# Optimization experiments

Measured on AMD Instinct MI355X. Metric: run time of the kernel, lower is better.

The kernel has to match this reference:

```python
import jax, jax.numpy as jnp
import numpy as np

V0, V1, V2 = 2000, 1500, 500   # diag / proc / med vocab sizes
D = 256                        # emb_dim
T = 16                         # visits per patient (query and memory)
P = 512                        # memory-bank patients
LD, LP, LM = 24, 16, 24        # codes per visit per type
PAD = V0 + V1 + V2             # padding row index (zeroed)
THRESH = 0.8
EPS = 1e-6


def setup_inputs() -> dict:
    key = jax.random.key(0)
    ks = jax.random.split(key, 16)
    inp = {
        "q_diag": jax.random.randint(ks[0], (T, LD), 0, V0),
        "q_proc": jax.random.randint(ks[1], (T, LP), 0, V1),
        "q_med": jax.random.randint(ks[2], (T, LM), 0, V2),
        "mem_diag": jax.random.randint(ks[3], (P, T, LD), 0, V0),
        "mem_proc": jax.random.randint(ks[4], (P, T, LP), 0, V1),
        "mem_med": jax.random.randint(ks[5], (P, T, LM), 0, V2),
        "emb": (jax.random.normal(ks[6], (PAD + 1, D)) * 0.05).at[PAD].set(0.0),
        "Wih": jax.random.normal(ks[7], (3 * D, D)) * 0.05,
        "Whh": jax.random.normal(ks[8], (3 * D, D)) * 0.05,
        "bih": jax.random.normal(ks[9], (3 * D,)) * 0.05,
        "bhh": jax.random.normal(ks[10], (3 * D,)) * 0.05,
        "W2": jax.random.normal(ks[11], (D, D)) * 0.05,
        "b2": jax.random.normal(ks[12], (D,)) * 0.05,
        "Wo": jax.random.normal(ks[13], (V2, D)) * 0.05,
        "bo": jax.random.normal(ks[14], (V2,)) * 0.05,
        "k": 16,
    }
    return inp


def _run_gru(x, Wih, Whh, bih, bhh):
    # x: [B, T, D]; torch nn.GRU gate order: r, z, n
    xT = jnp.swapaxes(x, 0, 1)                      # [T, B, D]
    gx = xT @ Wih.T + bih                           # [T, B, 3D]
    h0 = jnp.zeros(x.shape[:1] + x.shape[2:], x.dtype)  # [B, D]

    def step(h, gx_t):
        gh = h @ Whh.T + bhh
        xr, xz, xn = jnp.split(gx_t, 3, axis=-1)
        hr, hz, hn = jnp.split(gh, 3, axis=-1)
        r = jax.nn.sigmoid(xr + hr)
        z = jax.nn.sigmoid(xz + hz)
        n = jnp.tanh(xn + r * hn)
        h_new = (1.0 - z) * n + z * h
        return h_new, h_new

    _, hs = jax.lax.scan(step, h0, gx)
    return jnp.swapaxes(hs, 0, 1)                   # [B, T, D]


def _encode_visits(diag, proc, med, emb, Wih, Whh, bih, bhh, W2, b2):
    # diag/proc/med: [B, T, L*] int. Returns encoders for visits 1..T-1: [B, T-1, D].
    e_d = emb[diag].sum(axis=2)                     # [B, T, D]
    e_p = emb[proc + V0].sum(axis=2)
    e_m = emb[med + V0 + V1].sum(axis=2)
    e_nomed = e_d + e_p                             # current visit excludes meds
    e_full = e_nomed + e_m                          # history visits include meds
    h = _run_gru(e_full, Wih, Whh, bih, bhh)        # [B, T, D]
    # attn_g = softmax over size-1 axis == 1 exactly, so encoder_1 drops out.
    terms = jnp.tanh(h @ W2.T + b2) * e_full        # [B, T, D]
    c = jnp.cumsum(terms, axis=1)                   # prefix context sums
    return c[:, :-1] + e_nomed[:, 1:]               # enc_i = c_{i-1..} + current_i


def reference(q_diag, q_proc, q_med, mem_diag, mem_proc, mem_med,
              emb, Wih, Whh, bih, bhh, W2, b2, Wo, bo, k):
    gru = (Wih, Whh, bih, bhh)
    # Memory bank: every prefix encoder of every memory patient -> [P*(T-1), D]
    M = _encode_visits(mem_diag, mem_proc, mem_med, emb, *gru, W2, b2)
    M = M.reshape(-1, D)
    # Query patient prefix encoders -> [T-1, D]
    Q = _encode_visits(q_diag[None], q_proc[None], q_med[None], emb, *gru, W2, b2)[0]
    # Cosine similarity (torch CosineSimilarity, eps=1e-6)
    qn = jnp.maximum(jnp.linalg.norm(Q, axis=-1, keepdims=True), EPS)
    mn = jnp.maximum(jnp.linalg.norm(M, axis=-1, keepdims=True), EPS)
    sims = (Q / qn) @ (M / mn).T                    # [T-1, Nmem]
    vals, idx = jax.lax.top_k(sims, k)              # [T-1, k]
    w = jnp.where(vals > THRESH, vals, 0.0)         # threshold mask
    gathered = M[idx]                               # [T-1, k, D]
    out = Q + jnp.einsum("qk,qkd->qd", w, gathered) # weighted gather-sum
    return jax.nn.sigmoid(out @ Wo.T + bo)          # [T-1, V2]
```

## Files before the change

kernel.cpp:

```cpp
#include <hip/hip_runtime.h>
#include <math.h>

constexpr int V0_ = 2000, V1_ = 1500, V2_ = 500;
constexpr int D_ = 256, T_ = 16, P_ = 512;
constexpr int LD_ = 24, LP_ = 16, LM_ = 24;
constexpr int NPAT = P_ + 1;
constexpr int NV   = NPAT * T_;
constexpr int NM   = P_ * (T_ - 1);
constexpr int NQ   = T_ - 1;
constexpr int NROWS = NPAT * NQ;
constexpr float THRESH_ = 0.8f;
constexpr float EPS_ = 1e-6f;

__device__ __forceinline__ float sigmoidf_(float x) { return 1.0f / (1.0f + expf(-x)); }

#define BLO(u) __uint_as_float((u) << 16)
#define BHI(u) __uint_as_float((u) & 0xffff0000u)

__global__ void embed_kernel(const int* __restrict__ qd, const int* __restrict__ qp,
                             const int* __restrict__ qm, const int* __restrict__ md,
                             const int* __restrict__ mp, const int* __restrict__ mm,
                             const float* __restrict__ emb,
                             float* __restrict__ e_nomed, float* __restrict__ e_full) {
  int b = blockIdx.x;
  int p = b / T_, t = b % T_;
  int tid = threadIdx.x;
  __shared__ int codes[64];
  if (tid < 64) {
    int c;
    if (tid < LD_) {
      c = (p < P_) ? md[(p * T_ + t) * LD_ + tid] : qd[t * LD_ + tid];
    } else if (tid < LD_ + LP_) {
      int i = tid - LD_;
      c = ((p < P_) ? mp[(p * T_ + t) * LP_ + i] : qp[t * LP_ + i]) + V0_;
    } else {
      int i = tid - LD_ - LP_;
      c = ((p < P_) ? mm[(p * T_ + t) * LM_ + i] : qm[t * LM_ + i]) + V0_ + V1_;
    }
    codes[tid] = c;
  }
  __syncthreads();
  float s0 = 0.f, s1 = 0.f;
  #pragma unroll 8
  for (int i = 0; i < LD_ + LP_; ++i) s0 += emb[codes[i] * D_ + tid];
  #pragma unroll 8
  for (int i = LD_ + LP_; i < 64; ++i) s1 += emb[codes[i] * D_ + tid];
  e_nomed[(size_t)b * D_ + tid] = s0;
  e_full[(size_t)b * D_ + tid]  = s0 + s1;
}

#define BM 128
#define BN 64
#define BK 32
__global__ void gemm_nt_bias(const float* __restrict__ A, const float* __restrict__ B,
                             const float* __restrict__ bias, float* __restrict__ C,
                             int M, int N, int nct) {
  const int K = 256;
  __shared__ float As[BK][BM + 5];
  __shared__ float Bs[BK][BN + 5];
  int nb = gridDim.x;
  int b = blockIdx.x;
  int q = nb >> 3, r = nb & 7;
  int xcd = b & 7, i0 = b >> 3;
  int nbb = (xcd < r) ? (xcd * (q + 1) + i0) : (r * (q + 1) + (xcd - r) * q + i0);
  int rt = nbb / nct, ct = nbb - rt * nct;
  int r0 = rt * BM;
  int c0 = ct * BN;
  int tid = threadIdx.x;
  int tx = tid & 15, ty = tid >> 4;
  float acc[8][4];
  #pragma unroll
  for (int i = 0; i < 8; ++i)
    #pragma unroll
    for (int j = 0; j < 4; ++j) acc[i][j] = 0.f;

  for (int k0 = 0; k0 < K; k0 += BK) {
    #pragma unroll
    for (int i = 0; i < 4; ++i) {
      int flat = i * 256 + tid;
      int rr = flat >> 3;
      int kq = flat & 7;
      float4 v = make_float4(0.f, 0.f, 0.f, 0.f);
      if (r0 + rr < M) v = *(const float4*)(A + (size_t)(r0 + rr) * K + k0 + kq * 4);
      As[kq * 4 + 0][rr] = v.x; As[kq * 4 + 1][rr] = v.y;
      As[kq * 4 + 2][rr] = v.z; As[kq * 4 + 3][rr] = v.w;
    }
    #pragma unroll
    for (int i = 0; i < 2; ++i) {
      int flat = i * 256 + tid;
      int rr = flat >> 3;
      int kq = flat & 7;
      float4 v = *(const float4*)(B + (size_t)(c0 + rr) * K + k0 + kq * 4);
      Bs[kq * 4 + 0][rr] = v.x; Bs[kq * 4 + 1][rr] = v.y;
      Bs[kq * 4 + 2][rr] = v.z; Bs[kq * 4 + 3][rr] = v.w;
    }
    __syncthreads();
    #pragma unroll
    for (int kk = 0; kk < BK; ++kk) {
      float4 a0 = *(const float4*)&As[kk][ty * 8];
      float4 a1 = *(const float4*)&As[kk][ty * 8 + 4];
      float4 bv = *(const float4*)&Bs[kk][tx * 4];
      float av[8] = {a0.x, a0.y, a0.z, a0.w, a1.x, a1.y, a1.z, a1.w};
      float bw[4] = {bv.x, bv.y, bv.z, bv.w};
      #pragma unroll
      for (int i = 0; i < 8; ++i)
        #pragma unroll
        for (int j = 0; j < 4; ++j) acc[i][j] = fmaf(av[i], bw[j], acc[i][j]);
    }
    __syncthreads();
  }
  float bv0 = bias[c0 + tx * 4 + 0], bv1 = bias[c0 + tx * 4 + 1];
  float bv2 = bias[c0 + tx * 4 + 2], bv3 = bias[c0 + tx * 4 + 3];
  #pragma unroll
  for (int i = 0; i < 8; ++i) {
    int rr = r0 + ty * 8 + i;
    if (rr < M) {
      float4 o = make_float4(acc[i][0] + bv0, acc[i][1] + bv1,
                             acc[i][2] + bv2, acc[i][3] + bv3);
      *(float4*)(C + (size_t)rr * N + c0 + tx * 4) = o;
    }
  }
}

__global__ void pack_whh(const float* __restrict__ Whh, uint4* __restrict__ Wp) {
  int b = blockIdx.x;
  int e8 = b / 3, g = b - e8 * 3;
  int d = threadIdx.x;
  const float* src = Whh + (size_t)(g * 256 + d) * 256 + e8 * 8;
  unsigned rbits[8];
  #pragma unroll
  for (int j = 0; j < 8; ++j) {
    unsigned u = __float_as_uint(src[j]);
    rbits[j] = (u + 0x7fffu + ((u >> 16) & 1u)) >> 16;
  }
  uint4 o;
  o.x = rbits[0] | (rbits[1] << 16);
  o.y = rbits[2] | (rbits[3] << 16);
  o.z = rbits[4] | (rbits[5] << 16);
  o.w = rbits[6] | (rbits[7] << 16);
  Wp[(size_t)b * 256 + d] = o;
}

__global__ __launch_bounds__(1024) void gru_all(const float* __restrict__ gx,
                                                const uint4* __restrict__ Wp,
                                                const float* __restrict__ bhh,
                                                float* __restrict__ hs_all) {
  int tid = threadIdx.x;
  int d = tid & 255;
  int qt = tid >> 8;
  int p0 = blockIdx.x * 3;
  __shared__ float hL[3][D_];
  __shared__ float part[4][3][3][D_];
  if (qt == 0) { hL[0][d] = 0.f; hL[1][d] = 0.f; hL[2][d] = 0.f; }
  float brd = bhh[d], bzd = bhh[D_ + d], bnd = bhh[2 * D_ + d];
  __syncthreads();

  const uint4* wbase = Wp + d;
  for (int t = 0; t < T_; ++t) {
    float ar[3] = {0.f, 0.f, 0.f}, az[3] = {0.f, 0.f, 0.f}, an[3] = {0.f, 0.f, 0.f};
    int e80 = qt << 3;
    #pragma unroll 4
    for (int e8 = e80; e8 < e80 + 8; ++e8) {
      const uint4* wp = wbase + (size_t)(e8 * 3) * 256;
      uint4 w0 = wp[0];
      uint4 w1 = wp[256];
      uint4 w2 = wp[512];
      #pragma unroll
      for (int i = 0; i < 3; ++i) {
        float4 ha = *(const float4*)&hL[i][e8 << 3];
        float4 hb = *(const float4*)&hL[i][(e8 << 3) + 4];
        ar[i] = fmaf(ha.x, BLO(w0.x), ar[i]); ar[i] = fmaf(ha.y, BHI(w0.x), ar[i]);
        ar[i] = fmaf(ha.z, BLO(w0.y), ar[i]); ar[i] = fmaf(ha.w, BHI(w0.y), ar[i]);
        ar[i] = fmaf(hb.x, BLO(w0.z), ar[i]); ar[i] = fmaf(hb.y, BHI(w0.z), ar[i]);
        ar[i] = fmaf(hb.z, BLO(w0.w), ar[i]); ar[i] = fmaf(hb.w, BHI(w0.w), ar[i]);
        az[i] = fmaf(ha.x, BLO(w1.x), az[i]); az[i] = fmaf(ha.y, BHI(w1.x), az[i]);
        az[i] = fmaf(ha.z, BLO(w1.y), az[i]); az[i] = fmaf(ha.w, BHI(w1.y), az[i]);
        az[i] = fmaf(hb.x, BLO(w1.z), az[i]); az[i] = fmaf(hb.y, BHI(w1.z), az[i]);
        az[i] = fmaf(hb.z, BLO(w1.w), az[i]); az[i] = fmaf(hb.w, BHI(w1.w), az[i]);
        an[i] = fmaf(ha.x, BLO(w2.x), an[i]); an[i] = fmaf(ha.y, BHI(w2.x), an[i]);
        an[i] = fmaf(ha.z, BLO(w2.y), an[i]); an[i] = fmaf(ha.w, BHI(w2.y), an[i]);
        an[i] = fmaf(hb.x, BLO(w2.z), an[i]); an[i] = fmaf(hb.y, BHI(w2.z), an[i]);
        an[i] = fmaf(hb.z, BLO(w2.w), an[i]); an[i] = fmaf(hb.w, BHI(w2.w), an[i]);
      }
    }
    #pragma unroll
    for (int i = 0; i < 3; ++i) {
      part[qt][i][0][d] = ar[i];
      part[qt][i][1][d] = az[i];
      part[qt][i][2][d] = an[i];
    }
    __syncthreads();
    if (tid < 768) {
      int i = tid >> 8;
      int p = p0 + i;
      const float* gxp = gx + (size_t)(p * T_ + t) * 768;
      float arf = part[0][i][0][d] + part[1][i][0][d] + part[2][i][0][d] + part[3][i][0][d];
      float azf = part[0][i][1][d] + part[1][i][1][d] + part[2][i][1][d] + part[3][i][1][d];
      float anf = part[0][i][2][d] + part[1][i][2][d] + part[2][i][2][d] + part[3][i][2][d];
      float r = sigmoidf_(gxp[d] + brd + arf);
      float z = sigmoidf_(gxp[D_ + d] + bzd + azf);
      float n = tanhf(gxp[2 * D_ + d] + r * (anf + bnd));
      float hn = (1.f - z) * n + z * hL[i][d];
      hL[i][d] = hn;
      hs_all[(size_t)(p * T_ + t) * D_ + d] = hn;
    }
    __syncthreads();
  }
}

__global__ void enc_kernel(const float* __restrict__ tmp, const float* __restrict__ e_full,
                           const float* __restrict__ e_nomed, float* __restrict__ enc,
                           float* __restrict__ norms) {
  int p = blockIdx.x, d = threadIdx.x;
  __shared__ float red[4];
  float acc = 0.f;
  for (int t = 0; t < NQ; ++t) {
    size_t vi = (size_t)(p * T_ + t) * D_ + d;
    acc += tanhf(tmp[vi]) * e_full[vi];
    float ev = acc + e_nomed[(size_t)(p * T_ + t + 1) * D_ + d];
    int row = p * NQ + t;
    enc[(size_t)row * D_ + d] = ev;
    float s = ev * ev;
    #pragma unroll
    for (int off = 32; off > 0; off >>= 1) s += __shfl_down(s, off, 64);
    if ((d & 63) == 0) red[d >> 6] = s;
    __syncthreads();
    if (d == 0) norms[row] = fmaxf(sqrtf(red[0] + red[1] + red[2] + red[3]), EPS_);
    __syncthreads();
  }
}

__global__ void sims_kernel(const float* __restrict__ enc, const float* __restrict__ norms,
                            float* __restrict__ sims) {
  int q = blockIdx.y;
  int m = blockIdx.x * 256 + threadIdx.x;
  __shared__ float qs[D_];
  qs[threadIdx.x] = enc[(size_t)(NM + q) * D_ + threadIdx.x];
  __syncthreads();
  const float* mrow = enc + (size_t)m * D_;
  float dot = 0.f;
  #pragma unroll 8
  for (int e = 0; e < D_; e += 4) {
    float4 a = *(const float4*)(qs + e);
    float4 b = *(const float4*)(mrow + e);
    dot += a.x * b.x + a.y * b.y + a.z * b.z + a.w * b.w;
  }
  sims[(size_t)q * NM + m] = dot / (norms[NM + q] * norms[m]);
}

#define CAP 4096
__global__ void topk_gather(const float* __restrict__ sims, const float* __restrict__ enc,
                            const int* __restrict__ kptr, float* __restrict__ outq) {
  int q = blockIdx.x, tid = threadIdx.x;
  __shared__ int cnt;
  __shared__ float cv[CAP];
  __shared__ int ci[CAP];
  __shared__ float selv[64];
  __shared__ int seli[64];
  __shared__ float rv[256];
  __shared__ int ri[256];
  if (tid == 0) cnt = 0;
  __syncthreads();
  const float* sq = sims + (size_t)q * NM;
  for (int j = tid; j < NM; j += 256) {
    float v = sq[j];
    if (v > THRESH_) {
      int slot = atomicAdd(&cnt, 1);
      if (slot < CAP) { cv[slot] = v; ci[slot] = j; }
    }
  }
  __syncthreads();
  int k = kptr[0];
  if (k > 64) k = 64;
  if (k < 0) k = 0;
  int n = cnt; if (n > CAP) n = CAP;
  int nsel;
  if (n <= k) {
    nsel = n;
    if (tid < n) { selv[tid] = cv[tid]; seli[tid] = ci[tid]; }
  } else {
    nsel = k;
    for (int it = 0; it < k; ++it) {
      float best = -3e38f; int bslot = -1;
      for (int j = tid; j < n; j += 256) {
        float v = cv[j];
        if (v > best) { best = v; bslot = j; }
        else if (v == best && bslot >= 0 && ci[j] < ci[bslot]) { bslot = j; }
      }
      rv[tid] = best; ri[tid] = bslot;
      __syncthreads();
      for (int off = 128; off > 0; off >>= 1) {
        if (tid < off) {
          float v2 = rv[tid + off]; int s2 = ri[tid + off];
          if (s2 >= 0 && (ri[tid] < 0 || v2 > rv[tid] ||
                          (v2 == rv[tid] && ci[s2] < ci[ri[tid]]))) {
            rv[tid] = v2; ri[tid] = s2;
          }
        }
        __syncthreads();
      }
      if (tid == 0) {
        int s = ri[0];
        selv[it] = rv[0]; seli[it] = ci[s];
        cv[s] = -3e38f;
      }
      __syncthreads();
    }
  }
  __syncthreads();
  float o = enc[(size_t)(NM + q) * D_ + tid];
  for (int j = 0; j < nsel; ++j)
    o += selv[j] * enc[(size_t)seli[j] * D_ + tid];
  outq[(size_t)q * D_ + tid] = o;
}

__global__ void out_kernel(const float* __restrict__ outq, const float* __restrict__ Wo,
                           const float* __restrict__ bo, float* __restrict__ out) {
  int q = blockIdx.y;
  int v = blockIdx.x * 256 + threadIdx.x;
  __shared__ float qs[D_];
  qs[threadIdx.x] = outq[(size_t)q * D_ + threadIdx.x];
  __syncthreads();
  if (v >= V2_) return;
  const float* wr = Wo + (size_t)v * D_;
  float dot = bo[v];
  #pragma unroll 8
  for (int e = 0; e < D_; e += 4) {
    float4 a = *(const float4*)(qs + e);
    float4 b = *(const float4*)(wr + e);
    dot += a.x * b.x + a.y * b.y + a.z * b.z + a.w * b.w;
  }
  out[(size_t)q * V2_ + v] = 1.f / (1.f + expf(-dot));
}

extern "C" void kernel_launch(void* const* d_in, const int* in_sizes, int n_in,
                              void* d_out, int out_size, void* d_ws, size_t ws_size,
                              hipStream_t stream) {
  const int* qd = (const int*)d_in[0];
  const int* qp = (const int*)d_in[1];
  const int* qm = (const int*)d_in[2];
  const int* md = (const int*)d_in[3];
  const int* mp = (const int*)d_in[4];
  const int* mm = (const int*)d_in[5];
  const float* emb = (const float*)d_in[6];
  const float* Wih = (const float*)d_in[7];
  const float* Whh = (const float*)d_in[8];
  const float* bih = (const float*)d_in[9];
  const float* bhh = (const float*)d_in[10];
  const float* W2  = (const float*)d_in[11];
  const float* b2  = (const float*)d_in[12];
  const float* Wo  = (const float*)d_in[13];
  const float* bo  = (const float*)d_in[14];
  const int* kptr  = (const int*)d_in[15];
  float* out = (float*)d_out;
  (void)in_sizes; (void)n_in; (void)out_size; (void)ws_size;

  char* ws = (char*)d_ws;
  size_t off = 0;
  auto alloc = [&](size_t nfloats) {
    float* pp = (float*)(ws + off);
    off += ((nfloats * sizeof(float) + 255) & ~(size_t)255);
    return pp;
  };
  float* e_full  = alloc((size_t)NV * D_);
  float* e_nomed = alloc((size_t)NV * D_);
  float* gx      = alloc((size_t)NV * 768);
  float* hs_all  = alloc((size_t)NV * D_);
  float* tmp     = alloc((size_t)NV * D_);
  float* enc     = alloc((size_t)NROWS * D_);
  float* norms   = alloc(NROWS);
  float* sims    = alloc((size_t)NQ * NM);
  float* outq    = alloc((size_t)NQ * D_);
  uint4* Wp      = (uint4*)alloc((size_t)96 * 256 * 4);

  embed_kernel<<<NV, 256, 0, stream>>>(qd, qp, qm, md, mp, mm, emb, e_nomed, e_full);

  pack_whh<<<96, 256, 0, stream>>>(Whh, Wp);

  {
    int nrt = (NV + BM - 1) / BM, nct = 768 / BN;
    gemm_nt_bias<<<nrt * nct, 256, 0, stream>>>(e_full, Wih, bih, gx, NV, 768, nct);
  }

  gru_all<<<NPAT / 3, 1024, 0, stream>>>(gx, Wp, bhh, hs_all);

  {
    int nrt = (NV + BM - 1) / BM, nct = 256 / BN;
    gemm_nt_bias<<<nrt * nct, 256, 0, stream>>>(hs_all, W2, b2, tmp, NV, 256, nct);
  }

  enc_kernel<<<NPAT, 256, 0, stream>>>(tmp, e_full, e_nomed, enc, norms);
  sims_kernel<<<dim3(NM / 256, NQ), 256, 0, stream>>>(enc, norms, sims);
  topk_gather<<<NQ, 256, 0, stream>>>(sims, enc, kptr, outq);
  out_kernel<<<dim3((V2_ + 255) / 256, NQ), 256, 0, stream>>>(outq, Wo, bo, out);
}
```

Before: 362.3 us.

## Keep packed Whh slices resident in registers across GRU timesteps

The GRU kernel drops from 1024 to 512 threads per block. Each thread now preloads its 16x3 packed bf16 Whh uint4 slices into registers once, instead of re-reading them from global memory on every timestep. The cross-thread partial reduction shrinks from four quarters to two halves, and the half-0 threads also finish the third patient's gate update. The cost is heavy register pressure (192 VGPRs just for weights), possible spilling, and less parallelism per block, traded against removing repeated global weight loads.

New measurement: 477.6 us. 31.8% more time.

```diff
diff --git a/kernel.cpp b/kernel.cpp
--- a/kernel.cpp
+++ b/kernel.cpp
@@ -141,34 +141,44 @@
   Wp[(size_t)b * 256 + d] = o;
 }
 
-__global__ __launch_bounds__(1024) void gru_all(const float* __restrict__ gx,
-                                                const uint4* __restrict__ Wp,
-                                                const float* __restrict__ bhh,
-                                                float* __restrict__ hs_all) {
+__global__ __launch_bounds__(512, 2) void gru_all(const float* __restrict__ gx,
+                                                  const uint4* __restrict__ Wp,
+                                                  const float* __restrict__ bhh,
+                                                  float* __restrict__ hs_all) {
   int tid = threadIdx.x;
   int d = tid & 255;
-  int qt = tid >> 8;
+  int hf = tid >> 8;
   int p0 = blockIdx.x * 3;
   __shared__ float hL[3][D_];
-  __shared__ float part[4][3][3][D_];
-  if (qt == 0) { hL[0][d] = 0.f; hL[1][d] = 0.f; hL[2][d] = 0.f; }
+  __shared__ float part[2][3][3][D_];
+  if (hf == 0) { hL[0][d] = 0.f; hL[1][d] = 0.f; hL[2][d] = 0.f; }
   float brd = bhh[d], bzd = bhh[D_ + d], bnd = bhh[2 * D_ + d];
-  __syncthreads();
-
-  const uint4* wbase = Wp + d;
+
+  uint4 wr[16], wz[16], wn[16];
+  {
+    const uint4* wb = Wp + d;
+    #pragma unroll
+    for (int j = 0; j < 16; ++j) {
+      int e8 = hf * 16 + j;
+      wr[j] = wb[(size_t)(e8 * 3 + 0) * 256];
+      wz[j] = wb[(size_t)(e8 * 3 + 1) * 256];
+      wn[j] = wb[(size_t)(e8 * 3 + 2) * 256];
+    }
+  }
+  __syncthreads();
+
   for (int t = 0; t < T_; ++t) {
     float ar[3] = {0.f, 0.f, 0.f}, az[3] = {0.f, 0.f, 0.f}, an[3] = {0.f, 0.f, 0.f};
-    int e80 = qt << 3;
-    #pragma unroll 4
-    for (int e8 = e80; e8 < e80 + 8; ++e8) {
-      const uint4* wp = wbase + (size_t)(e8 * 3) * 256;
-      uint4 w0 = wp[0];
-      uint4 w1 = wp[256];
-      uint4 w2 = wp[512];
+    #pragma unroll
+    for (int j = 0; j < 16; ++j) {
+      int eb = (hf * 16 + j) << 3;
+      uint4 w0 = wr[j];
+      uint4 w1 = wz[j];
+      uint4 w2 = wn[j];
       #pragma unroll
       for (int i = 0; i < 3; ++i) {
-        float4 ha = *(const float4*)&hL[i][e8 << 3];
-        float4 hb = *(const float4*)&hL[i][(e8 << 3) + 4];
+        float4 ha = *(const float4*)&hL[i][eb];
+        float4 hb = *(const float4*)&hL[i][eb + 4];
         ar[i] = fmaf(ha.x, BLO(w0.x), ar[i]); ar[i] = fmaf(ha.y, BHI(w0.x), ar[i]);
         ar[i] = fmaf(ha.z, BLO(w0.y), ar[i]); ar[i] = fmaf(ha.w, BHI(w0.y), ar[i]);
         ar[i] = fmaf(hb.x, BLO(w0.z), ar[i]); ar[i] = fmaf(hb.y, BHI(w0.z), ar[i]);
@@ -185,18 +195,32 @@
     }
     #pragma unroll
     for (int i = 0; i < 3; ++i) {
-      part[qt][i][0][d] = ar[i];
-      part[qt][i][1][d] = az[i];
-      part[qt][i][2][d] = an[i];
-    }
-    __syncthreads();
-    if (tid < 768) {
-      int i = tid >> 8;
+      part[hf][i][0][d] = ar[i];
+      part[hf][i][1][d] = az[i];
+      part[hf][i][2][d] = an[i];
+    }
+    __syncthreads();
+    {
+      int i = hf;
       int p = p0 + i;
       const float* gxp = gx + (size_t)(p * T_ + t) * 768;
-      float arf = part[0][i][0][d] + part[1][i][0][d] + part[2][i][0][d] + part[3][i][0][d];
-      float azf = part[0][i][1][d] + part[1][i][1][d] + part[2][i][1][d] + part[3][i][1][d];
-      float anf = part[0][i][2][d] + part[1][i][2][d] + part[2][i][2][d] + part[3][i][2][d];
+      float arf = part[0][i][0][d] + part[1][i][0][d];
+      float azf = part[0][i][1][d] + part[1][i][1][d];
+      float anf = part[0][i][2][d] + part[1][i][2][d];
+      float r = sigmoidf_(gxp[d] + brd + arf);
+      float z = sigmoidf_(gxp[D_ + d] + bzd + azf);
+      float n = tanhf(gxp[2 * D_ + d] + r * (anf + bnd));
+      float hn = (1.f - z) * n + z * hL[i][d];
+      hL[i][d] = hn;
+      hs_all[(size_t)(p * T_ + t) * D_ + d] = hn;
+    }
+    if (hf == 0) {
+      int i = 2;
+      int p = p0 + 2;
+      const float* gxp = gx + (size_t)(p * T_ + t) * 768;
+      float arf = part[0][i][0][d] + part[1][i][0][d];
+      float azf = part[0][i][1][d] + part[1][i][1][d];
+      float anf = part[0][i][2][d] + part[1][i][2][d];
       float r = sigmoidf_(gxp[d] + brd + arf);
       float z = sigmoidf_(gxp[D_ + d] + bzd + azf);
       float n = tanhf(gxp[2 * D_ + d] + r * (anf + bnd));
@@ -382,7 +406,7 @@
     gemm_nt_bias<<<nrt * nct, 256, 0, stream>>>(e_full, Wih, bih, gx, NV, 768, nct);
   }
 
-  gru_all<<<NPAT / 3, 1024, 0, stream>>>(gx, Wp, bhh, hs_all);
+  gru_all<<<NPAT / 3, 512, 0, stream>>>(gx, Wp, bhh, hs_all);
 
   {
     int nrt = (NV + BM - 1) / BM, nct = 256 / BN;
```
